# Kernel tuning notes

Measured on AMD Instinct MI355X. Metric: run time of the kernel, lower is better.

## Reference

```python
import jax, jax.numpy as jnp
import numpy as np

B, T, D, K = 16, 1024, 256, 1024

def setup_inputs() -> dict:
    key = jax.random.key(0)
    k1, k2 = jax.random.split(key)
    x = jax.random.normal(k1, (B, T, D), dtype=jnp.float32)
    codebook = jax.random.normal(k2, (K, D), dtype=jnp.float32)
    precision = jnp.ones((1,), dtype=jnp.float32)
    return {"x": x, "codebook": codebook, "precision": precision}

def reference(x, codebook, precision):
    # score[b,t,k] = -precision * ||x[b,t] - codebook[k]||^2
    x_sq = jnp.sum(x * x, axis=-1, keepdims=True)            # [B,T,1]
    c_sq = jnp.sum(codebook * codebook, axis=-1)             # [K]
    xc = jnp.einsum('btd,kd->btk', x, codebook)              # [B,T,K]
    dist_sq = x_sq - 2.0 * xc + c_sq                         # [B,T,K]
    return -precision[0] * dist_sq
```

## Files before the change

kernel.cpp:

```cpp
#include <hip/hip_runtime.h>
#include <hip/hip_bf16.h>
#include <cstdint>

#define M_ROWS 16384
#define D_DIM  256
#define K_ROWS 1024

typedef __bf16 bf16x8 __attribute__((ext_vector_type(8)));
typedef __bf16 bf16x4 __attribute__((ext_vector_type(4)));
typedef float  f32x4  __attribute__((ext_vector_type(4)));

__device__ inline void load_lds16(const void* g, void* l) {
  __builtin_amdgcn_global_load_lds(
      (const __attribute__((address_space(1))) void*)(uintptr_t)g,
      (__attribute__((address_space(3))) void*)(uintptr_t)l,
      16, 0, 0);
}

__global__ __launch_bounds__(256) void prep_kernel(
    const float* __restrict__ x, const float* __restrict__ cb,
    __bf16* __restrict__ xbf, __bf16* __restrict__ cbf,
    float* __restrict__ xsq, float* __restrict__ csq)
{
  const int row = blockIdx.x * 4 + (threadIdx.x >> 6);
  const int l   = threadIdx.x & 63;

  const float* src;
  __bf16* dst;
  float* nrm;
  if (row < M_ROWS) {
    src = x   + (size_t)row * D_DIM;
    dst = xbf + (size_t)row * D_DIM;
    nrm = xsq + row;
  } else {
    const int r = row - M_ROWS;
    src = cb  + (size_t)r * D_DIM;
    dst = cbf + (size_t)r * D_DIM;
    nrm = csq + r;
  }

  const float4 v = reinterpret_cast<const float4*>(src)[l];
  float s = v.x * v.x + v.y * v.y + v.z * v.z + v.w * v.w;

  bf16x4 h;
  h[0] = (__bf16)v.x; h[1] = (__bf16)v.y; h[2] = (__bf16)v.z; h[3] = (__bf16)v.w;
  *reinterpret_cast<bf16x4*>(dst + l * 4) = h;

  #pragma unroll
  for (int o = 32; o > 0; o >>= 1) s += __shfl_xor(s, o);
  if (l == 0) *nrm = s;
}

__global__ __launch_bounds__(256) void gemm_kernel(
    const __bf16* __restrict__ xbf, const __bf16* __restrict__ cbf,
    const float* __restrict__ xsq, const float* __restrict__ csq,
    const float* __restrict__ prec, float* __restrict__ out)
{
  __shared__ __bf16 At[128 * 32];
  __shared__ __bf16 Bt[128 * 32];

  const int tid = threadIdx.x;
  const int w   = tid >> 6;
  const int l   = tid & 63;
  const int wr  = w >> 1;
  const int wc  = w & 1;

  const int bx   = blockIdx.x;
  const int tc   = bx & 7;
  const int tr   = bx >> 3;
  const int row0 = tr * 128;
  const int col0 = tc * 128;

  const int srow = tid >> 2;
  const int scol = (tid & 3) * 8;
  const __bf16* gA = xbf + (size_t)(row0 + srow) * D_DIM + scol;
  const __bf16* gB = cbf + (size_t)(col0 + srow) * D_DIM + scol;
  char* ldsA = (char*)At + w * 1024;
  char* ldsB = (char*)Bt + w * 1024;

  f32x4 acc[4][4] = {};

  const int lr = l & 15;
  const int lk = (l >> 4) * 8;

  for (int k0 = 0; k0 < D_DIM; k0 += 32) {
    load_lds16(gA + k0,                       ldsA);
    load_lds16(gA + k0 + (size_t)64 * D_DIM,  ldsA + 4096);
    load_lds16(gB + k0,                       ldsB);
    load_lds16(gB + k0 + (size_t)64 * D_DIM,  ldsB + 4096);
    __syncthreads();

    bf16x8 af[4], bfm[4];
    #pragma unroll
    for (int f = 0; f < 4; ++f) {
      af[f]  = *reinterpret_cast<const bf16x8*>(&At[(wr * 64 + f * 16 + lr) * 32 + lk]);
      bfm[f] = *reinterpret_cast<const bf16x8*>(&Bt[(wc * 64 + f * 16 + lr) * 32 + lk]);
    }

    #pragma unroll
    for (int i = 0; i < 4; ++i)
      #pragma unroll
      for (int j = 0; j < 4; ++j)
        acc[i][j] = __builtin_amdgcn_mfma_f32_16x16x32_bf16(af[i], bfm[j], acc[i][j], 0, 0, 0);

    __syncthreads();
  }

  const float p  = prec[0];
  const int   lq = l >> 4;
  #pragma unroll
  for (int j = 0; j < 4; ++j) {
    const int colg = col0 + wc * 64 + j * 16 + lr;
    const float cs = csq[colg];
    #pragma unroll
    for (int i = 0; i < 4; ++i) {
      #pragma unroll
      for (int r = 0; r < 4; ++r) {
        const int rowg = row0 + wr * 64 + i * 16 + lq * 4 + r;
        const float xs = xsq[rowg];
        out[(size_t)rowg * K_ROWS + colg] = -p * (xs - 2.0f * acc[i][j][r] + cs);
      }
    }
  }
}

extern "C" void kernel_launch(void* const* d_in, const int* in_sizes, int n_in,
                              void* d_out, int out_size, void* d_ws, size_t ws_size,
                              hipStream_t stream) {
  const float* x    = (const float*)d_in[0];
  const float* cb   = (const float*)d_in[1];
  const float* prec = (const float*)d_in[2];
  float* out = (float*)d_out;

  char* ws = (char*)d_ws;
  __bf16* xbf = (__bf16*)ws;
  __bf16* cbf = (__bf16*)(ws + 8388608);
  float*  xsq = (float*)(ws + 8912896);
  float*  csq = (float*)(ws + 8978432);

  prep_kernel<<<(M_ROWS + K_ROWS) / 4, 256, 0, stream>>>(x, cb, xbf, cbf, xsq, csq);
  gemm_kernel<<<(M_ROWS / 128) * (K_ROWS / 128), 256, 0, stream>>>(xbf, cbf, xsq, csq, prec, out);
}
```

Baseline: 39.57 us.

## Register-prefetch K=64 tiles with swizzled LDS, remap tiles, vectorize output stores

Replaces direct global-to-LDS loads with register-staged loads that prefetch the next K=64 slice while computing the current one. LDS tiles double to 128x64 and use an XOR swizzle to avoid bank conflicts. Blocks are remapped so consecutive blocks share a codebook column tile. MFMA operands are swapped so each lane holds four consecutive output columns, which allows 16-byte vector stores and float4 csq loads. The cost is higher register pressure from the prefetch buffers and more index arithmetic.

```diff
diff --git a/kernel.cpp b/kernel.cpp
--- a/kernel.cpp
+++ b/kernel.cpp
@@ -9,13 +9,6 @@
 typedef __bf16 bf16x8 __attribute__((ext_vector_type(8)));
 typedef __bf16 bf16x4 __attribute__((ext_vector_type(4)));
 typedef float  f32x4  __attribute__((ext_vector_type(4)));
-
-__device__ inline void load_lds16(const void* g, void* l) {
-  __builtin_amdgcn_global_load_lds(
-      (const __attribute__((address_space(1))) void*)(uintptr_t)g,
-      (__attribute__((address_space(3))) void*)(uintptr_t)l,
-      16, 0, 0);
-}
 
 __global__ __launch_bounds__(256) void prep_kernel(
     const float* __restrict__ x, const float* __restrict__ cb,
@@ -56,8 +49,8 @@
     const float* __restrict__ xsq, const float* __restrict__ csq,
     const float* __restrict__ prec, float* __restrict__ out)
 {
-  __shared__ __bf16 At[128 * 32];
-  __shared__ __bf16 Bt[128 * 32];
+  __shared__ __bf16 At[128 * 64];
+  __shared__ __bf16 Bt[128 * 64];
 
   const int tid = threadIdx.x;
   const int w   = tid >> 6;
@@ -66,60 +59,86 @@
   const int wc  = w & 1;
 
   const int bx   = blockIdx.x;
-  const int tc   = bx & 7;
-  const int tr   = bx >> 3;
+  const int tile = (bx & 7) * 128 + (bx >> 3);
+  const int tr   = tile >> 3;
+  const int tc   = tile & 7;
   const int row0 = tr * 128;
   const int col0 = tc * 128;
 
-  const int srow = tid >> 2;
-  const int scol = (tid & 3) * 8;
-  const __bf16* gA = xbf + (size_t)(row0 + srow) * D_DIM + scol;
-  const __bf16* gB = cbf + (size_t)(col0 + srow) * D_DIM + scol;
-  char* ldsA = (char*)At + w * 1024;
-  char* ldsB = (char*)Bt + w * 1024;
+  const int srow = tid >> 3;
+  const int sg   = tid & 7;
+  const int swg  = (sg ^ (srow & 7)) * 16;
+  const __bf16* gA = xbf + (size_t)(row0 + srow) * D_DIM + sg * 8;
+  const __bf16* gB = cbf + (size_t)(col0 + srow) * D_DIM + sg * 8;
+  char* const wA = (char*)At + srow * 128 + swg;
+  char* const wB = (char*)Bt + srow * 128 + swg;
 
   f32x4 acc[4][4] = {};
 
   const int lr = l & 15;
-  const int lk = (l >> 4) * 8;
+  const int lk = l >> 4;
 
-  for (int k0 = 0; k0 < D_DIM; k0 += 32) {
-    load_lds16(gA + k0,                       ldsA);
-    load_lds16(gA + k0 + (size_t)64 * D_DIM,  ldsA + 4096);
-    load_lds16(gB + k0,                       ldsB);
-    load_lds16(gB + k0 + (size_t)64 * D_DIM,  ldsB + 4096);
+  bf16x8 ra[4], rb[4];
+  #pragma unroll
+  for (int n = 0; n < 4; ++n) {
+    ra[n] = *reinterpret_cast<const bf16x8*>(gA + (size_t)(n * 32) * D_DIM);
+    rb[n] = *reinterpret_cast<const bf16x8*>(gB + (size_t)(n * 32) * D_DIM);
+  }
+
+  #pragma unroll
+  for (int t = 0; t < 4; ++t) {
+    #pragma unroll
+    for (int n = 0; n < 4; ++n) {
+      *reinterpret_cast<bf16x8*>(wA + n * 4096) = ra[n];
+      *reinterpret_cast<bf16x8*>(wB + n * 4096) = rb[n];
+    }
     __syncthreads();
 
-    bf16x8 af[4], bfm[4];
-    #pragma unroll
-    for (int f = 0; f < 4; ++f) {
-      af[f]  = *reinterpret_cast<const bf16x8*>(&At[(wr * 64 + f * 16 + lr) * 32 + lk]);
-      bfm[f] = *reinterpret_cast<const bf16x8*>(&Bt[(wc * 64 + f * 16 + lr) * 32 + lk]);
+    if (t < 3) {
+      const int k0 = (t + 1) * 64;
+      #pragma unroll
+      for (int n = 0; n < 4; ++n) {
+        ra[n] = *reinterpret_cast<const bf16x8*>(gA + (size_t)(n * 32) * D_DIM + k0);
+        rb[n] = *reinterpret_cast<const bf16x8*>(gB + (size_t)(n * 32) * D_DIM + k0);
+      }
     }
 
     #pragma unroll
-    for (int i = 0; i < 4; ++i)
+    for (int ks = 0; ks < 2; ++ks) {
+      bf16x8 af[4], bfm[4];
       #pragma unroll
-      for (int j = 0; j < 4; ++j)
-        acc[i][j] = __builtin_amdgcn_mfma_f32_16x16x32_bf16(af[i], bfm[j], acc[i][j], 0, 0, 0);
-
+      for (int f = 0; f < 4; ++f) {
+        const int rar = wr * 64 + f * 16 + lr;
+        af[f] = *reinterpret_cast<const bf16x8*>(
+            (const char*)At + rar * 128 + ((ks * 64 + lk * 16) ^ ((rar & 7) << 4)));
+        const int rbr = wc * 64 + f * 16 + lr;
+        bfm[f] = *reinterpret_cast<const bf16x8*>(
+            (const char*)Bt + rbr * 128 + ((ks * 64 + lk * 16) ^ ((rbr & 7) << 4)));
+      }
+      #pragma unroll
+      for (int i = 0; i < 4; ++i)
+        #pragma unroll
+        for (int j = 0; j < 4; ++j)
+          acc[i][j] = __builtin_amdgcn_mfma_f32_16x16x32_bf16(bfm[j], af[i], acc[i][j], 0, 0, 0);
+    }
     __syncthreads();
   }
 
-  const float p  = prec[0];
-  const int   lq = l >> 4;
+  const float p = prec[0];
   #pragma unroll
-  for (int j = 0; j < 4; ++j) {
-    const int colg = col0 + wc * 64 + j * 16 + lr;
-    const float cs = csq[colg];
+  for (int i = 0; i < 4; ++i) {
+    const int rowg = row0 + wr * 64 + i * 16 + lr;
+    const float xs = xsq[rowg];
+    float* orow = out + (size_t)rowg * K_ROWS;
     #pragma unroll
-    for (int i = 0; i < 4; ++i) {
+    for (int j = 0; j < 4; ++j) {
+      const int colg = col0 + wc * 64 + j * 16 + lk * 4;
+      const f32x4 cs = *reinterpret_cast<const f32x4*>(&csq[colg]);
+      f32x4 v;
       #pragma unroll
-      for (int r = 0; r < 4; ++r) {
-        const int rowg = row0 + wr * 64 + i * 16 + lq * 4 + r;
-        const float xs = xsq[rowg];
-        out[(size_t)rowg * K_ROWS + colg] = -p * (xs - 2.0f * acc[i][j][r] + cs);
-      }
+      for (int r = 0; r < 4; ++r)
+        v[r] = -p * (xs - 2.0f * acc[i][j][r] + cs[r]);
+      *reinterpret_cast<f32x4*>(&orow[colg]) = v;
     }
   }
 }
```

Result: faster. 33.61 us (-15.1%).
